# Optimization experiments

Measured on AMD Instinct MI355X. Metric: run time of the kernel, lower is better.

The kernel has to match this reference:

```python
import jax, jax.numpy as jnp
import numpy as np

DG, K, PAD = 4, 3, 1  # deformable_groups, kernel_size, padding=(K-1)//2
K2 = K * K


def setup_inputs() -> dict:
    key = jax.random.key(0)
    k1, k2, k3, k4 = jax.random.split(key, 4)
    B, C, H, W, O = 2, 256, 200, 200, 256
    x = jax.random.normal(k1, (B, C, H, W), jnp.float32)
    # conv_offset_mask params (zero-init in the module; small random here so the
    # deformable gather is actually exercised with nonzero offsets/masks)
    w_om = jax.random.normal(k2, (DG * 3 * K2, C, K, K), jnp.float32) * 0.01
    b_om = jax.random.normal(k3, (DG * 3 * K2,), jnp.float32) * 0.1
    # ModulatedDeformConv weight (bias=False)
    w_dcn = jax.random.normal(k4, (O, C, K, K), jnp.float32) * (1.0 / np.sqrt(C * K2))
    return {"x": x, "w_om": w_om, "b_om": b_om, "w_dcn": w_dcn}


def _mdcn(x, offset, mask, weight):
    """Modulated deformable conv v2, stride 1, padding PAD, no bias.
    offset: [B, DG*2*K2, H, W] interpreted (per DCNv2 CUDA kernel) as
            [B, DG, K2, 2(dy,dx), H, W]; mask: [B, DG*K2, H, W]."""
    B, C, H, W = x.shape
    Cg = C // DG
    off = offset.reshape(B, DG, K2, 2, H, W)
    dy, dx = off[:, :, :, 0], off[:, :, :, 1]          # [B,DG,K2,H,W]
    m = mask.reshape(B, DG, K2, H, W)
    ki = jnp.repeat(jnp.arange(K), K)                  # kernel row per tap
    kj = jnp.tile(jnp.arange(K), K)                    # kernel col per tap
    hh = jnp.arange(H, dtype=x.dtype)
    ww = jnp.arange(W, dtype=x.dtype)
    # absolute sampling positions [B,DG,K2,H,W]
    py = hh[None, None, None, :, None] - PAD + ki[None, None, :, None, None] + dy
    px = ww[None, None, None, None, :] - PAD + kj[None, None, :, None, None] + dx
    y0 = jnp.floor(py)
    x0 = jnp.floor(px)
    wy = py - y0
    wx = px - x0
    y0i = y0.astype(jnp.int32)
    x0i = x0.astype(jnp.int32)
    xf = x.reshape(B, DG, Cg, H * W)

    def gather(yi, xi):
        valid = ((yi >= 0) & (yi < H) & (xi >= 0) & (xi < W)).astype(x.dtype)
        idx = jnp.clip(yi, 0, H - 1) * W + jnp.clip(xi, 0, W - 1)
        g = jnp.take_along_axis(xf, idx.reshape(B, DG, 1, K2 * H * W), axis=3)
        return g.reshape(B, DG, Cg, K2, H, W) * valid[:, :, None]

    # bilinear sample with zero padding outside, [B,DG,Cg,K2,H,W]
    v = (gather(y0i, x0i) * ((1 - wy) * (1 - wx))[:, :, None]
         + gather(y0i, x0i + 1) * ((1 - wy) * wx)[:, :, None]
         + gather(y0i + 1, x0i) * (wy * (1 - wx))[:, :, None]
         + gather(y0i + 1, x0i + 1) * (wy * wx)[:, :, None])
    v = v * m[:, :, None]
    wr = weight.reshape(-1, DG, Cg, K2)  # [O,DG,Cg,K2]
    return jnp.einsum('ogck,bgckhw->bohw', wr, v)


def reference(x, w_om, b_om, w_dcn):
    om = jax.lax.conv_general_dilated(
        x, w_om, (1, 1), ((PAD, PAD), (PAD, PAD)),
        dimension_numbers=('NCHW', 'OIHW', 'NCHW')) + b_om[None, :, None, None]
    o1, o2, mask = jnp.split(om, 3, axis=1)
    offset = jnp.concatenate([o1, o2], axis=1)
    mask = jax.nn.sigmoid(mask)
    return jax.nn.relu(_mdcn(x, offset, mask, w_dcn))
```

## Files before the change

### kernel.cpp

```cpp
#include <hip/hip_runtime.h>
#include <math.h>

#define HH 200
#define WW 200
#define CIN 256
#define OMCH 108
#define OCH 256
#define NPIX (HH*WW)

typedef _Float16 f16x8 __attribute__((ext_vector_type(8)));
typedef float floatx4 __attribute__((ext_vector_type(4)));

static __device__ __forceinline__ unsigned short f16bits(float v) {
    _Float16 h = (_Float16)v;
    return __builtin_bit_cast(unsigned short, h);
}
static __device__ __forceinline__ _Float16 f16lo(unsigned int u) {
    return __builtin_bit_cast(_Float16, (unsigned short)(u & 0xffffu));
}
static __device__ __forceinline__ _Float16 f16hi(unsigned int u) {
    return __builtin_bit_cast(_Float16, (unsigned short)(u >> 16));
}

static __device__ __forceinline__ int xcd_swizzle(int orig, int nwg) {
    int q = nwg >> 3, r = nwg & 7;
    int x = orig & 7, rank = orig >> 3;
    int base = (x < r) ? x * (q + 1) : r * (q + 1) + (x - r) * q;
    return base + rank;
}

__global__ __launch_bounds__(256) void transpose_x(const float* __restrict__ x,
                                                   unsigned short* __restrict__ xT) {
    __shared__ __align__(16) unsigned short st[64][264];
    int t = threadIdx.x;
    int blk = blockIdx.x;
    int b = blk / 625, pix0 = (blk % 625) * 64;
    const float* xb = x + (size_t)b * CIN * NPIX + pix0;
    int p = t & 63, oct = t >> 6;

    for (int c32 = 0; c32 < CIN; c32 += 32) {
        int c = c32 + oct * 8;
        union { unsigned short u[8]; float4 f; } pk;
#pragma unroll
        for (int i = 0; i < 8; i++)
            pk.u[i] = f16bits(xb[(size_t)(c + i) * NPIX + p]);
        *(float4*)&st[p][c] = pk.f;
    }
    __syncthreads();
    int p2 = t >> 2, qo = t & 3;
    unsigned short* dst = xT + ((size_t)b * NPIX + pix0 + p2) * CIN + qo * 64;
#pragma unroll
    for (int j = 0; j < 8; j++)
        *(float4*)(dst + j * 8) = *(const float4*)&st[p2][qo * 64 + j * 8];
}

__global__ void prep_wom(const float* __restrict__ w, unsigned short* __restrict__ wom3) {
    int i = blockIdx.x * 256 + threadIdx.x;
    int slice = i >> 12, rem = i & 4095;
    int oc = rem >> 5, qj = rem & 31;
    int ks = slice & 1, it = slice >> 1;
    int tap = it >> 2, c64 = it & 3;
    int c = c64 * 64 + ks * 32 + qj;
    float v = (oc < OMCH) ? w[(size_t)oc * 2304 + c * 9 + tap] : 0.f;
    wom3[i] = f16bits(v);
}

__global__ void prep_wdcn(const float* __restrict__ w, unsigned short* __restrict__ wt3) {
    int i = blockIdx.x * 256 + threadIdx.x;
    int slice = i >> 13, rem = i & 8191;
    int oc = rem >> 5, qj = rem & 31;
    int ks = slice & 1, gk = slice >> 1;
    int g = gk / 9, kk = gk % 9;
    int cin = g * 64 + ks * 32 + qj;
    wt3[i] = f16bits(w[(size_t)oc * 2304 + cin * 9 + kk]);
}

__global__ __launch_bounds__(512, 6) void om_mfma(const unsigned short* __restrict__ xT,
                                                  const unsigned short* __restrict__ wom3,
                                                  const float* __restrict__ bom,
                                                  float* __restrict__ om) {
    __shared__ __align__(16) unsigned short vbuf[2][128][72];

    int t = threadIdx.x;
    int p4 = t >> 2;
    int c4 = t & 3;
    int lane = t & 63, n16 = t & 15, quad = lane >> 4, wv = t >> 6;
    int ocbase = (wv & 3) * 32;
    int ph = (wv >> 2) * 64;

    int gp0 = xcd_swizzle(blockIdx.x, 625) * 128;
    int sp = gp0 + p4;
    int sb = (sp >= NPIX) ? 1 : 0;
    int srem = sp - sb * NPIX;
    int sh = srem / WW, sw = srem % WW;
    const unsigned short* xtb = xT + (size_t)sb * NPIX * CIN;

    floatx4 acc[2][4];
#pragma unroll
    for (int i = 0; i < 2; i++)
#pragma unroll
        for (int j = 0; j < 4; j++) acc[i][j] = (floatx4){0.f, 0.f, 0.f, 0.f};

    {
        int h2 = sh - 1, w2 = sw - 1;
        bool valid = ((unsigned)h2 < (unsigned)HH) && ((unsigned)w2 < (unsigned)WW);
        float4 fa = {0.f,0.f,0.f,0.f}, fb = {0.f,0.f,0.f,0.f};
        if (valid) {
            const unsigned short* src = xtb + (size_t)(h2 * WW + w2) * CIN + c4 * 8;
            fa = *(const float4*)src;
            fb = *(const float4*)(src + 32);
        }
        *(float4*)&vbuf[0][p4][c4 * 8]      = fa;
        *(float4*)&vbuf[0][p4][32 + c4 * 8] = fb;
    }
    __syncthreads();

    for (int it = 0; it < 36; it++) {
        int cur = it & 1;
        bool have = (it < 35);

        float4 nfa = {0.f,0.f,0.f,0.f}, nfb = {0.f,0.f,0.f,0.f};
        if (have) {
            int itn = it + 1;
            int tapn = itn >> 2, c0n = (itn & 3) << 6;
            int h2 = sh + tapn / 3 - 1, w2 = sw + tapn % 3 - 1;
            bool valid = ((unsigned)h2 < (unsigned)HH) && ((unsigned)w2 < (unsigned)WW);
            if (valid) {
                const unsigned short* src = xtb + (size_t)(h2 * WW + w2) * CIN + c0n + c4 * 8;
                nfa = *(const float4*)src;
                nfb = *(const float4*)(src + 32);
            }
        }

#pragma unroll
        for (int ks = 0; ks < 2; ks++) {
            f16x8 bf0 = *(const f16x8*)&vbuf[cur][ph + n16     ][ks * 32 + quad * 8];
            f16x8 bf1 = *(const f16x8*)&vbuf[cur][ph + 16 + n16][ks * 32 + quad * 8];
            f16x8 bf2 = *(const f16x8*)&vbuf[cur][ph + 32 + n16][ks * 32 + quad * 8];
            f16x8 bf3 = *(const f16x8*)&vbuf[cur][ph + 48 + n16][ks * 32 + quad * 8];
#pragma unroll
            for (int oi = 0; oi < 2; oi++) {
                f16x8 a = *(const f16x8*)&wom3[(size_t)(it * 2 + ks) * 4096
                                               + (ocbase + oi * 16 + n16) * 32 + quad * 8];
                acc[oi][0] = __builtin_amdgcn_mfma_f32_16x16x32_f16(a, bf0, acc[oi][0], 0, 0, 0);
                acc[oi][1] = __builtin_amdgcn_mfma_f32_16x16x32_f16(a, bf1, acc[oi][1], 0, 0, 0);
                acc[oi][2] = __builtin_amdgcn_mfma_f32_16x16x32_f16(a, bf2, acc[oi][2], 0, 0, 0);
                acc[oi][3] = __builtin_amdgcn_mfma_f32_16x16x32_f16(a, bf3, acc[oi][3], 0, 0, 0);
            }
        }

        if (have) {
            *(float4*)&vbuf[cur ^ 1][p4][c4 * 8]      = nfa;
            *(float4*)&vbuf[cur ^ 1][p4][32 + c4 * 8] = nfb;
            __syncthreads();
        }
    }

#pragma unroll
    for (int oi = 0; oi < 2; oi++) {
        int oc0 = ocbase + oi * 16 + quad * 4;
        if (oc0 < OMCH) {
#pragma unroll
            for (int pt = 0; pt < 4; pt++) {
                int fp = gp0 + ph + pt * 16 + n16;
                int bq = (fp >= NPIX) ? 1 : 0;
                int rem = fp - bq * NPIX;
#pragma unroll
                for (int r = 0; r < 4; r++) {
                    int occ = oc0 + r;
                    if (occ < OMCH)
                        om[((size_t)(bq * OMCH + occ)) * NPIX + rem] = acc[oi][pt][r] + bom[occ];
                }
            }
        }
    }
}

__global__ __launch_bounds__(512, 6) void dcn_mfma(const unsigned short* __restrict__ xT,
                                                   const float* __restrict__ om,
                                                   const unsigned short* __restrict__ wt3,
                                                   float* __restrict__ out) {
    __shared__ unsigned int iPk[36 * 64];
    __shared__ uint2        wPk[36 * 64];
    __shared__ __align__(16) unsigned short vbuf[2][64][72];

    int t = threadIdx.x;
    int l = t & 63;
    int oct = t >> 6;
    int p8 = l >> 3;
    int chunk = l & 7;
    int mypix = oct * 8 + p8;
    int n16 = t & 15, quad = l >> 4;
    int ocbase = oct * 32;

    int gp0 = xcd_swizzle(blockIdx.x, 1250) * 64;
    int b = gp0 / NPIX;
    int pix0 = gp0 - b * NPIX;
    const unsigned short* xtb = xT + (size_t)b * NPIX * CIN;
    const float* omb = om + (size_t)b * OMCH * NPIX;

    for (int r = t; r < 36 * 64; r += 512) {
        int gk = r >> 6, p = r & 63;
        int g = gk / 9, kk = gk % 9;
        int ki = kk / 3, kj = kk % 3;
        int pp = pix0 + p;
        int hh = pp / WW, ww2 = pp % WW;
        float dy = omb[(size_t)(g * 18 + 2 * kk    ) * NPIX + pp];
        float dx = omb[(size_t)(g * 18 + 2 * kk + 1) * NPIX + pp];
        float mr = omb[(size_t)(72 + g * 9 + kk    ) * NPIX + pp];
        float m = 1.f / (1.f + __expf(-mr));
        float py = (float)(hh - 1 + ki) + dy;
        float px = (float)(ww2 - 1 + kj) + dx;
        float fy = floorf(py), fx = floorf(px);
        float wy = py - fy, wx = px - fx;
        int y0 = (int)fy, x0 = (int)fx, y1 = y0 + 1, x1 = x0 + 1;
        bool vy0 = (y0 >= 0) && (y0 < HH), vy1 = (y1 >= 0) && (y1 < HH);
        bool vx0 = (x0 >= 0) && (x0 < WW), vx1 = (x1 >= 0) && (x1 < WW);
        int cy0 = min(max(y0, 0), HH - 1), cy1 = min(max(y1, 0), HH - 1);
        int cx0 = min(max(x0, 0), WW - 1), cx1 = min(max(x1, 0), WW - 1);
        float w00 = (vy0 && vx0) ? (1.f - wy) * (1.f - wx) * m : 0.f;
        float w01 = (vy0 && vx1) ? (1.f - wy) * wx * m : 0.f;
        float w10 = (vy1 && vx0) ? wy * (1.f - wx) * m : 0.f;
        float w11 = (vy1 && vx1) ? wy * wx * m : 0.f;
        int i00 = cy0 * WW + cx0;
        unsigned int dx1 = (unsigned int)(cx1 - cx0);
        unsigned int dy1 = (unsigned int)(cy1 - cy0);
        iPk[r] = (unsigned int)i00 | (dx1 << 16) | (dy1 << 17);
        uint2 wp;
        wp.x = (unsigned int)f16bits(w00) | ((unsigned int)f16bits(w01) << 16);
        wp.y = (unsigned int)f16bits(w10) | ((unsigned int)f16bits(w11) << 16);
        wPk[r] = wp;
    }
    __syncthreads();

    floatx4 acc[2][4];
#pragma unroll
    for (int i = 0; i < 2; i++)
#pragma unroll
        for (int j = 0; j < 4; j++) acc[i][j] = (floatx4){0.f, 0.f, 0.f, 0.f};

    unsigned int ipNext; uint2 wpNext;

    {
        unsigned int ip = iPk[mypix];
        uint2 wp = wPk[mypix];
        int i00 = ip & 0xffff;
        int dx1 = (ip >> 16) & 1, dy1 = (ip >> 17) & 1;
        int i01 = i00 + dx1, i10 = i00 + dy1 * WW, i11 = i10 + dx1;
        const unsigned short* xg = xtb + chunk * 8;
        f16x8 c00 = *(const f16x8*)(xg + (size_t)i00 * CIN);
        f16x8 c01 = *(const f16x8*)(xg + (size_t)i01 * CIN);
        f16x8 c10 = *(const f16x8*)(xg + (size_t)i10 * CIN);
        f16x8 c11 = *(const f16x8*)(xg + (size_t)i11 * CIN);
        ipNext = iPk[64 + mypix];
        wpNext = wPk[64 + mypix];
        f16x8 v = c00 * f16lo(wp.x) + c01 * f16hi(wp.x)
                + c10 * f16lo(wp.y) + c11 * f16hi(wp.y);
        *(float4*)&vbuf[0][mypix][chunk * 8] = __builtin_bit_cast(float4, v);
    }
    __syncthreads();

    for (int gk = 0; gk < 36; gk++) {
        int cur = gk & 1;
        bool have = (gk < 35);

        _Float16 nw00, nw01, nw10, nw11;
        f16x8 n00, n01, n10, n11;
        if (have) {
            unsigned int ip = ipNext; uint2 wp = wpNext;
            int i00 = ip & 0xffff;
            int dx1 = (ip >> 16) & 1, dy1 = (ip >> 17) & 1;
            int i01 = i00 + dx1, i10 = i00 + dy1 * WW, i11 = i10 + dx1;
            const unsigned short* xg = xtb + ((gk + 1) / 9) * 64 + chunk * 8;
            n00 = *(const f16x8*)(xg + (size_t)i00 * CIN);
            n01 = *(const f16x8*)(xg + (size_t)i01 * CIN);
            n10 = *(const f16x8*)(xg + (size_t)i10 * CIN);
            n11 = *(const f16x8*)(xg + (size_t)i11 * CIN);
            nw00 = f16lo(wp.x); nw01 = f16hi(wp.x);
            nw10 = f16lo(wp.y); nw11 = f16hi(wp.y);
        }
        if (gk < 34) {
            ipNext = iPk[(gk + 2) * 64 + mypix];
            wpNext = wPk[(gk + 2) * 64 + mypix];
        }

#pragma unroll
        for (int ks = 0; ks < 2; ks++) {
            f16x8 bf0 = *(const f16x8*)&vbuf[cur][n16     ][ks * 32 + quad * 8];
            f16x8 bf1 = *(const f16x8*)&vbuf[cur][16 + n16][ks * 32 + quad * 8];
            f16x8 bf2 = *(const f16x8*)&vbuf[cur][32 + n16][ks * 32 + quad * 8];
            f16x8 bf3 = *(const f16x8*)&vbuf[cur][48 + n16][ks * 32 + quad * 8];
#pragma unroll
            for (int oi = 0; oi < 2; oi++) {
                f16x8 a = *(const f16x8*)&wt3[(size_t)(gk * 2 + ks) * 8192
                                              + (ocbase + oi * 16 + n16) * 32 + quad * 8];
                acc[oi][0] = __builtin_amdgcn_mfma_f32_16x16x32_f16(a, bf0, acc[oi][0], 0, 0, 0);
                acc[oi][1] = __builtin_amdgcn_mfma_f32_16x16x32_f16(a, bf1, acc[oi][1], 0, 0, 0);
                acc[oi][2] = __builtin_amdgcn_mfma_f32_16x16x32_f16(a, bf2, acc[oi][2], 0, 0, 0);
                acc[oi][3] = __builtin_amdgcn_mfma_f32_16x16x32_f16(a, bf3, acc[oi][3], 0, 0, 0);
            }
        }

        if (have) {
            f16x8 v = n00 * nw00 + n01 * nw01 + n10 * nw10 + n11 * nw11;
            *(float4*)&vbuf[cur ^ 1][mypix][chunk * 8] = __builtin_bit_cast(float4, v);
            __syncthreads();
        }
    }

#pragma unroll
    for (int oi = 0; oi < 2; oi++)
#pragma unroll
        for (int pt = 0; pt < 4; pt++) {
            int gpix = pix0 + pt * 16 + n16;
#pragma unroll
            for (int r = 0; r < 4; r++) {
                int oc = ocbase + oi * 16 + quad * 4 + r;
                out[((size_t)(b * OCH + oc)) * NPIX + gpix] = fmaxf(acc[oi][pt][r], 0.f);
            }
        }
}

extern "C" void kernel_launch(void* const* d_in, const int* in_sizes, int n_in,
                              void* d_out, int out_size, void* d_ws, size_t ws_size,
                              hipStream_t stream) {
    const float* x     = (const float*)d_in[0];
    const float* w_om  = (const float*)d_in[1];
    const float* b_om  = (const float*)d_in[2];
    const float* w_dcn = (const float*)d_in[3];
    float* out = (float*)d_out;

    char* ws = (char*)d_ws;
    float*          om   = (float*)(ws);
    unsigned short* xT   = (unsigned short*)(ws + 34560000);
    unsigned short* wom3 = (unsigned short*)(ws + 75520000);
    unsigned short* wt3  = (unsigned short*)(ws + 76109824);

    transpose_x<<<1250, 256, 0, stream>>>(x, xT);
    prep_wom   <<<1152, 256, 0, stream>>>(w_om, wom3);
    prep_wdcn  <<<2304, 256, 0, stream>>>(w_dcn, wt3);
    om_mfma    <<< 625, 512, 0, stream>>>(xT, wom3, b_om, om);
    dcn_mfma   <<<1250, 512, 0, stream>>>(xT, om, wt3, out);
}
```

Measured before the change: 397.8 us.

## Tile offset conv by half-rows with shared 3-row halo reuse across taps

```diff
diff --git a/kernel.cpp b/kernel.cpp
--- a/kernel.cpp
+++ b/kernel.cpp
@@ -79,21 +79,18 @@
                                                   const unsigned short* __restrict__ wom3,
                                                   const float* __restrict__ bom,
                                                   float* __restrict__ om) {
-    __shared__ __align__(16) unsigned short vbuf[2][128][72];
+    __shared__ __align__(16) unsigned short vtile[3][114][72];
 
     int t = threadIdx.x;
-    int p4 = t >> 2;
-    int c4 = t & 3;
-    int lane = t & 63, n16 = t & 15, quad = lane >> 4, wv = t >> 6;
+    int lane = t & 63, n16 = t & 15, quad = (lane >> 4) & 3, wv = t >> 6;
     int ocbase = (wv & 3) * 32;
-    int ph = (wv >> 2) * 64;
-
-    int gp0 = xcd_swizzle(blockIdx.x, 625) * 128;
-    int sp = gp0 + p4;
-    int sb = (sp >= NPIX) ? 1 : 0;
-    int srem = sp - sb * NPIX;
-    int sh = srem / WW, sw = srem % WW;
-    const unsigned short* xtb = xT + (size_t)sb * NPIX * CIN;
+    int wh = wv >> 2;
+
+    int bid = xcd_swizzle(blockIdx.x, 800);
+    int b = bid / 400, rem0 = bid - b * 400;
+    int h = rem0 >> 1, hf = rem0 & 1;
+    int c0 = hf * 100;
+    const unsigned short* xtb = xT + (size_t)b * NPIX * CIN;
 
     floatx4 acc[2][4];
 #pragma unroll
@@ -101,75 +98,69 @@
 #pragma unroll
         for (int j = 0; j < 4; j++) acc[i][j] = (floatx4){0.f, 0.f, 0.f, 0.f};
 
-    {
-        int h2 = sh - 1, w2 = sw - 1;
-        bool valid = ((unsigned)h2 < (unsigned)HH) && ((unsigned)w2 < (unsigned)WW);
-        float4 fa = {0.f,0.f,0.f,0.f}, fb = {0.f,0.f,0.f,0.f};
-        if (valid) {
-            const unsigned short* src = xtb + (size_t)(h2 * WW + w2) * CIN + c4 * 8;
-            fa = *(const float4*)src;
-            fb = *(const float4*)(src + 32);
-        }
-        *(float4*)&vbuf[0][p4][c4 * 8]      = fa;
-        *(float4*)&vbuf[0][p4][32 + c4 * 8] = fb;
-    }
-    __syncthreads();
-
-    for (int it = 0; it < 36; it++) {
-        int cur = it & 1;
-        bool have = (it < 35);
-
-        float4 nfa = {0.f,0.f,0.f,0.f}, nfb = {0.f,0.f,0.f,0.f};
-        if (have) {
-            int itn = it + 1;
-            int tapn = itn >> 2, c0n = (itn & 3) << 6;
-            int h2 = sh + tapn / 3 - 1, w2 = sw + tapn % 3 - 1;
-            bool valid = ((unsigned)h2 < (unsigned)HH) && ((unsigned)w2 < (unsigned)WW);
-            if (valid) {
-                const unsigned short* src = xtb + (size_t)(h2 * WW + w2) * CIN + c0n + c4 * 8;
-                nfa = *(const float4*)src;
-                nfb = *(const float4*)(src + 32);
-            }
-        }
-
-#pragma unroll
-        for (int ks = 0; ks < 2; ks++) {
-            f16x8 bf0 = *(const f16x8*)&vbuf[cur][ph + n16     ][ks * 32 + quad * 8];
-            f16x8 bf1 = *(const f16x8*)&vbuf[cur][ph + 16 + n16][ks * 32 + quad * 8];
-            f16x8 bf2 = *(const f16x8*)&vbuf[cur][ph + 32 + n16][ks * 32 + quad * 8];
-            f16x8 bf3 = *(const f16x8*)&vbuf[cur][ph + 48 + n16][ks * 32 + quad * 8];
-#pragma unroll
-            for (int oi = 0; oi < 2; oi++) {
-                f16x8 a = *(const f16x8*)&wom3[(size_t)(it * 2 + ks) * 4096
-                                               + (ocbase + oi * 16 + n16) * 32 + quad * 8];
-                acc[oi][0] = __builtin_amdgcn_mfma_f32_16x16x32_f16(a, bf0, acc[oi][0], 0, 0, 0);
-                acc[oi][1] = __builtin_amdgcn_mfma_f32_16x16x32_f16(a, bf1, acc[oi][1], 0, 0, 0);
-                acc[oi][2] = __builtin_amdgcn_mfma_f32_16x16x32_f16(a, bf2, acc[oi][2], 0, 0, 0);
-                acc[oi][3] = __builtin_amdgcn_mfma_f32_16x16x32_f16(a, bf3, acc[oi][3], 0, 0, 0);
-            }
-        }
-
-        if (have) {
-            *(float4*)&vbuf[cur ^ 1][p4][c4 * 8]      = nfa;
-            *(float4*)&vbuf[cur ^ 1][p4][32 + c4 * 8] = nfb;
-            __syncthreads();
-        }
-    }
-
+    for (int chunk = 0; chunk < 4; chunk++) {
+        if (chunk) __syncthreads();
+
+        for (int k = 0; k < 6; k++) {
+            int L = t + k * 512;
+            if (L < 2736) {
+                int r3 = L / 912, r2 = L - r3 * 912;
+                int cc = r2 >> 3, u16 = r2 & 7;
+                int gr = h - 1 + r3, gc = c0 - 1 + cc;
+                float4 v = {0.f, 0.f, 0.f, 0.f};
+                if ((unsigned)gr < (unsigned)HH && (unsigned)gc < (unsigned)WW && cc < 102)
+                    v = *(const float4*)(xtb + (size_t)(gr * WW + gc) * CIN + chunk * 64 + u16 * 8);
+                *(float4*)&vtile[r3][cc][u16 * 8] = v;
+            }
+        }
+        __syncthreads();
+
+#pragma unroll 3
+        for (int tap = 0; tap < 9; tap++) {
+            int r3 = tap / 3, dj = tap - r3 * 3;
+            int colb = dj + wh * 64 + n16;
+#pragma unroll
+            for (int ks = 0; ks < 2; ks++) {
+                int ch = ks * 32 + quad * 8;
+                f16x8 bf0 = *(const f16x8*)&vtile[r3][colb     ][ch];
+                f16x8 bf1 = *(const f16x8*)&vtile[r3][colb + 16][ch];
+                f16x8 bf2 = *(const f16x8*)&vtile[r3][colb + 32][ch];
+                const unsigned short* wb = wom3 + (size_t)((tap * 4 + chunk) * 2 + ks) * 4096
+                                           + (ocbase + n16) * 32 + quad * 8;
+                f16x8 a0 = *(const f16x8*)wb;
+                f16x8 a1 = *(const f16x8*)(wb + 512);
+                acc[0][0] = __builtin_amdgcn_mfma_f32_16x16x32_f16(a0, bf0, acc[0][0], 0, 0, 0);
+                acc[1][0] = __builtin_amdgcn_mfma_f32_16x16x32_f16(a1, bf0, acc[1][0], 0, 0, 0);
+                acc[0][1] = __builtin_amdgcn_mfma_f32_16x16x32_f16(a0, bf1, acc[0][1], 0, 0, 0);
+                acc[1][1] = __builtin_amdgcn_mfma_f32_16x16x32_f16(a1, bf1, acc[1][1], 0, 0, 0);
+                acc[0][2] = __builtin_amdgcn_mfma_f32_16x16x32_f16(a0, bf2, acc[0][2], 0, 0, 0);
+                acc[1][2] = __builtin_amdgcn_mfma_f32_16x16x32_f16(a1, bf2, acc[1][2], 0, 0, 0);
+                if (wh == 0) {
+                    f16x8 bf3 = *(const f16x8*)&vtile[r3][colb + 48][ch];
+                    acc[0][3] = __builtin_amdgcn_mfma_f32_16x16x32_f16(a0, bf3, acc[0][3], 0, 0, 0);
+                    acc[1][3] = __builtin_amdgcn_mfma_f32_16x16x32_f16(a1, bf3, acc[1][3], 0, 0, 0);
+                }
+            }
+        }
+    }
+
+    int hbase = h * WW + c0;
 #pragma unroll
     for (int oi = 0; oi < 2; oi++) {
         int oc0 = ocbase + oi * 16 + quad * 4;
         if (oc0 < OMCH) {
 #pragma unroll
-            for (int pt = 0; pt < 4; pt++) {
-                int fp = gp0 + ph + pt * 16 + n16;
-                int bq = (fp >= NPIX) ? 1 : 0;
-                int rem = fp - bq * NPIX;
-#pragma unroll
-                for (int r = 0; r < 4; r++) {
-                    int occ = oc0 + r;
-                    if (occ < OMCH)
-                        om[((size_t)(bq * OMCH + occ)) * NPIX + rem] = acc[oi][pt][r] + bom[occ];
+            for (int tile = 0; tile < 4; tile++) {
+                if (wh && tile == 3) continue;
+                int pl = (wh * 4 + tile) * 16 + n16;
+                if (pl < 100) {
+#pragma unroll
+                    for (int r = 0; r < 4; r++) {
+                        int oc = oc0 + r;
+                        if (oc < OMCH)
+                            om[((size_t)(b * OMCH + oc)) * NPIX + hbase + pl]
+                                = acc[oi][tile][r] + bom[oc];
+                    }
                 }
             }
         }
@@ -339,6 +330,6 @@
     transpose_x<<<1250, 256, 0, stream>>>(x, xT);
     prep_wom   <<<1152, 256, 0, stream>>>(w_om, wom3);
     prep_wdcn  <<<2304, 256, 0, stream>>>(w_dcn, wt3);
-    om_mfma    <<< 625, 512, 0, stream>>>(xT, wom3, b_om, om);
+    om_mfma    <<< 800, 512, 0, stream>>>(xT, wom3, b_om, om);
     dcn_mfma   <<<1250, 512, 0, stream>>>(xT, om, wt3, out);
 }
```

Measured after the change: 394.1 us. Within noise of the previous version (-0.9%).
